# Kernel optimization log

Measured on AMD Instinct MI355X. Metric: run time of the kernel, lower is better.

The kernel has to match this reference:

```python
import jax, jax.numpy as jnp
import numpy as np

B = 2048          # puzzles
E_PER = 1620      # 81 cells * 20 constraint neighbors
N = B * 81        # total nodes
NFEAT = 10


def _winit(key, fan_in, fan_out):
    s = (1.0 / np.sqrt(fan_in)).astype(np.float32) if isinstance(fan_in, np.ndarray) else 1.0 / np.sqrt(fan_in)
    return jax.random.uniform(key, (fan_in, fan_out), jnp.float32, -s, s)


def setup_inputs() -> dict:
    key = jax.random.key(0)
    ks = jax.random.split(key, 20)
    x = jax.random.normal(ks[0], (N, NFEAT), jnp.float32)
    # batched edge index [B, 2, E_PER]; values are global node ids
    edge_index = jax.random.randint(ks[1], (B, 2, E_PER), 0, N, dtype=jnp.int32)
    dims = [(NFEAT, 16), (16, 32), (32, 64), (64, 32), (32, 16)]
    params = {}
    for i, (ci, co) in enumerate(dims, start=1):
        params[f'W{i}'] = _winit(ks[2 * i], ci, co)
        params[f'b{i}'] = jnp.zeros((co,), jnp.float32)
    params['fW1'] = _winit(ks[14], 16, 16)
    params['fb1'] = jnp.zeros((16,), jnp.float32)
    params['fW2'] = _winit(ks[15], 16, 9)
    params['fb2'] = jnp.zeros((9,), jnp.float32)
    return {'x': x, 'edge_index': edge_index, **params}


def _gcn(h, W, b, src, dst, norm):
    # GCNConv: out[i] = sum_{j->i} norm_ij * (h_j W) + b   (self-loops included in src/dst)
    h = h @ W                                  # [N, Cout] small GEMM
    msg = h[src] * norm[:, None]               # gather + scale, [E+N, Cout]
    return jax.ops.segment_sum(msg, dst, num_segments=N) + b


def reference(x, edge_index, W1, b1, W2, b2, W3, b3, W4, b4, W5, b5, fW1, fb1, fW2, fb2):
    # replicate edge_index.permute(1,2,0).reshape(2,-1)
    ei = jnp.transpose(edge_index, (1, 2, 0)).reshape(2, -1)
    src, dst = ei[0], ei[1]
    # add self loops (PyG gcn_norm default)
    loop = jnp.arange(N, dtype=src.dtype)
    src = jnp.concatenate([src, loop])
    dst = jnp.concatenate([dst, loop])
    deg = jax.ops.segment_sum(jnp.ones(src.shape, x.dtype), dst, num_segments=N)
    dinv = jnp.where(deg > 0, jax.lax.rsqrt(jnp.maximum(deg, 1e-12)), 0.0)
    norm = dinv[src] * dinv[dst]               # shared across layers (same graph)
    h = jax.nn.relu(_gcn(x, W1, b1, src, dst, norm))
    h = jax.nn.relu(_gcn(h, W2, b2, src, dst, norm))
    h = jax.nn.relu(_gcn(h, W3, b3, src, dst, norm))
    h = jax.nn.relu(_gcn(h, W4, b4, src, dst, norm))
    h = jax.nn.relu(_gcn(h, W5, b5, src, dst, norm))
    h = h.reshape(-1, 16)
    h = jax.nn.relu(h @ fW1 + fb1)
    h = h @ fW2 + fb2
    return h.reshape(-1, 81, 9)
```

## Files before the change

### kernel.cpp

```cpp
#include <hip/hip_runtime.h>
#include <hip/hip_fp16.h>


#define NN    165888
#define NBAT  2048
#define EPER  1620
#define NEDGE (NBAT * EPER)
#define ETOT  (NEDGE + NN)
#define NBKT  648
#define NBLK  512
#define SLICE 20736
#define BCAP  6144


__device__ inline void blk_scan256(int val, int& excl, int& total, int* sw) {
  int lane = threadIdx.x & 63, w = threadIdx.x >> 6;
  int x = val;
#pragma unroll
  for (int off = 1; off < 64; off <<= 1) {
    int y = __shfl_up(x, off);
    if (lane >= off) x += y;
  }
  if (lane == 63) sw[w] = x;
  __syncthreads();
  int woff = 0;
  if (w > 0) woff = sw[0];
  if (w > 1) woff += sw[1];
  if (w > 2) woff += sw[2];
  total = sw[0] + sw[1] + sw[2] + sw[3];
  excl = woff + x - val;
}

__device__ inline void pbase_scan(const int* __restrict__ btot, int* pb, int* sw) {
  int t = threadIdx.x;
  int e0 = 0, e1 = 0, e2 = 0, s = 0;
  if (t < 216) {
    e0 = btot[3 * t]; e1 = btot[3 * t + 1]; e2 = btot[3 * t + 2];
    s = e0 + e1 + e2;
  }
  int excl, tot;
  blk_scan256(s, excl, tot, sw);
  if (t < 216) {
    pb[3 * t]     = excl;
    pb[3 * t + 1] = excl + e0;
    pb[3 * t + 2] = excl + e0 + e1;
  }
  __syncthreads();
}


__global__ __launch_bounds__(256) void k_count(const int* __restrict__ ei,
                                               int* __restrict__ counts) {
  __shared__ int cnt[NBKT];
  int t = threadIdx.x;
  for (int k = t; k < NBKT; k += 256) cnt[k] = 0;
  __syncthreads();
  int b0 = blockIdx.x * 4;
  for (int b = b0; b < b0 + 4; ++b) {
    const int* dstp = ei + (size_t)b * (2 * EPER) + EPER;
    for (int e = t; e < EPER; e += 256) atomicAdd(&cnt[dstp[e] >> 8], 1);
  }
  __syncthreads();
  for (int k = t; k < NBKT; k += 256) counts[blockIdx.x * NBKT + k] = cnt[k];
}

__global__ __launch_bounds__(256) void k_scan(const int* __restrict__ counts,
                                              int* __restrict__ basesT,
                                              int* __restrict__ btot) {
  int bkt = blockIdx.x, t = threadIdx.x;
  int a = counts[(2 * t)     * NBKT + bkt];
  int b = counts[(2 * t + 1) * NBKT + bkt];
  __shared__ int sw[4];
  int excl, tot;
  blk_scan256(a + b, excl, tot, sw);
  basesT[bkt * NBLK + 2 * t]     = excl;
  basesT[bkt * NBLK + 2 * t + 1] = excl + a;
  if (t == 255) btot[bkt] = tot;
}

__global__ __launch_bounds__(256) void k_scat(const int* __restrict__ ei,
                                              const int* __restrict__ basesT,
                                              const int* __restrict__ btot,
                                              unsigned int* __restrict__ pairs) {
  __shared__ int cur[NBKT];
  __shared__ int pb[NBKT];
  __shared__ int sw[4];
  pbase_scan(btot, pb, sw);
  int t = threadIdx.x;
  for (int k = t; k < NBKT; k += 256)
    cur[k] = pb[k] + basesT[k * NBLK + blockIdx.x];
  __syncthreads();
  int b0 = blockIdx.x * 4;
  for (int b = b0; b < b0 + 4; ++b) {
    const int* srcp = ei + (size_t)b * (2 * EPER);
    const int* dstp = srcp + EPER;
    for (int e = t; e < EPER; e += 256) {
      int d = dstp[e];
      unsigned int s = (unsigned int)srcp[e];
      int pos = atomicAdd(&cur[d >> 8], 1);
      pairs[pos] = s | ((unsigned int)(d & 255) << 24);
    }
  }
}

__global__ __launch_bounds__(256) void k_build(const unsigned int* __restrict__ pairs,
                                               const int* __restrict__ btot,
                                               const float* __restrict__ x,
                                               const float* __restrict__ W1,
                                               int* __restrict__ row_start,
                                               int* __restrict__ row_end,
                                               float* __restrict__ dinv,
                                               int* __restrict__ csr,
                                               __half* __restrict__ g0) {
  __shared__ int pb[NBKT];
  __shared__ int sw[4];
  __shared__ int cnt[256];
  __shared__ unsigned int sp[BCAP];
  __shared__ float sW[160];
  int bkt = blockIdx.x, t = threadIdx.x;
  cnt[t] = 0;
  if (t < 160) sW[t] = W1[t];
  pbase_scan(btot, pb, sw);
  int p0 = pb[bkt];
  int n  = btot[bkt];
  for (int k = t; k < n; k += 256) {
    unsigned int pr = pairs[p0 + k];
    if (k < BCAP) sp[k] = pr;
    atomicAdd(&cnt[pr >> 24], 1);
  }
  __syncthreads();
  int indeg = cnt[t];
  int excl, tot;
  blk_scan256(indeg, excl, tot, sw);
  int csrbase = p0 + bkt * 256;
  int rs   = csrbase + excl + t;
  int node = bkt * 256 + t;
  int d    = indeg + 1;
  float di = rsqrtf((float)d);
  row_start[node] = rs;
  row_end[node]   = rs + d;
  dinv[node] = di;
  csr[rs] = node;
  __syncthreads();
  cnt[t] = rs + 1;
  __syncthreads();
  for (int k = t; k < n; k += 256) {
    unsigned int pr = (k < BCAP) ? sp[k] : pairs[p0 + k];
    int pos = atomicAdd(&cnt[pr >> 24], 1);
    csr[pos] = (int)(pr & 0x00FFFFFFu);
  }
  float r[10];
#pragma unroll
  for (int k = 0; k < 10; ++k) r[k] = x[(size_t)node * 10 + k];
  float acc[16];
#pragma unroll
  for (int j = 0; j < 16; ++j) acc[j] = 0.0f;
#pragma unroll
  for (int k = 0; k < 10; ++k) {
    float rv = r[k];
#pragma unroll
    for (int j = 0; j < 16; ++j) acc[j] = fmaf(rv, sW[k * 16 + j], acc[j]);
  }
  __half* op = g0 + (size_t)node * 16;
  union { int4 v; __half2 h[4]; } pk;
#pragma unroll
  for (int half8 = 0; half8 < 2; ++half8) {
#pragma unroll
    for (int j = 0; j < 4; ++j)
      pk.h[j] = __floats2half2_rn(acc[half8 * 8 + 2 * j] * di,
                                  acc[half8 * 8 + 2 * j + 1] * di);
    *(int4*)(op + half8 * 8) = pk.v;
  }
}


template <int C, int EPI>
__device__ inline float4 agg_core_h(const __half* __restrict__ g,
                                    const int* __restrict__ csr,
                                    int rs, int re, int q, int gl) {
  constexpr int LG = C / 4;
  float4 acc = make_float4(0.f, 0.f, 0.f, 0.f);
  const __half* gq = g + (size_t)q * 4;
  int iters = 0;
  for (int p = rs; p < re; p += EPI) {
    ++iters;
    int m[EPI / LG];
#pragma unroll
    for (int u = 0; u < EPI / LG; ++u) {
      int idx = p + u * LG + q;
      m[u] = csr[idx < re ? idx : re - 1];
    }
    float2 v[EPI];
#pragma unroll
    for (int j = 0; j < EPI; ++j) {
      int s = __shfl(m[j / LG], gl + (j % LG));
      v[j] = *(const float2*)(gq + (size_t)s * C);
    }
#pragma unroll
    for (int j = 0; j < EPI; ++j) {
      const __half2* hp = (const __half2*)&v[j];
      float2 lo = __half22float2(hp[0]);
      float2 hi = __half22float2(hp[1]);
      acc.x += lo.x; acc.y += lo.y; acc.z += hi.x; acc.w += hi.y;
    }
  }
  float dups = (float)(iters * EPI - (re - rs));
  int slast = csr[re - 1];
  float2 vl = *(const float2*)(gq + (size_t)slast * C);
  const __half2* hp = (const __half2*)&vl;
  float2 lo = __half22float2(hp[0]);
  float2 hi = __half22float2(hp[1]);
  acc.x = fmaf(-dups, lo.x, acc.x);
  acc.y = fmaf(-dups, lo.y, acc.y);
  acc.z = fmaf(-dups, hi.x, acc.z);
  acc.w = fmaf(-dups, hi.y, acc.w);
  return acc;
}


__global__ __launch_bounds__(256) void k_agg_ep16(const __half* __restrict__ g,
                                                  const int* __restrict__ row_start,
                                                  const int* __restrict__ row_end,
                                                  const int* __restrict__ csr,
                                                  const float* __restrict__ dinv,
                                                  const float* __restrict__ bias,
                                                  __half* __restrict__ out) {
  constexpr int LG = 4, NPB = 64, SPB = SLICE / NPB;
  int t  = threadIdx.x;
  int q  = t & (LG - 1);
  int bi = blockIdx.x;
  int vb = (bi & 7) * SPB + (bi >> 3);
  int i  = vb * NPB + t / LG;
  int gl = (t & 63) & ~(LG - 1);
  float4 acc = agg_core_h<16, 16>(g, csr, row_start[i], row_end[i], q, gl);
  float di = dinv[i];
  float4 bb = *(const float4*)(bias + q * 4);
  acc.x = fmaxf(fmaf(di, acc.x, bb.x), 0.f) * di;
  acc.y = fmaxf(fmaf(di, acc.y, bb.y), 0.f) * di;
  acc.z = fmaxf(fmaf(di, acc.z, bb.z), 0.f) * di;
  acc.w = fmaxf(fmaf(di, acc.w, bb.w), 0.f) * di;
  union { int2 v; __half2 h[2]; } pk;
  pk.h[0] = __floats2half2_rn(acc.x, acc.y);
  pk.h[1] = __floats2half2_rn(acc.z, acc.w);
  *(int2*)(out + (size_t)i * 16 + q * 4) = pk.v;
}


__global__ __launch_bounds__(256) void k_agg_g2(const __half* __restrict__ g,
                                                const int* __restrict__ row_start,
                                                const int* __restrict__ row_end,
                                                const int* __restrict__ csr,
                                                const float* __restrict__ dinv,
                                                const float* __restrict__ W2,
                                                const float* __restrict__ b2,
                                                __half* __restrict__ out) {
  constexpr int CI = 16, CO = 32, LG = 4, NPB = 64, SPB = SLICE / NPB, RP = 20;
  __shared__ float sW[CI * CO];
  __shared__ float sB[CO];
  __shared__ float rows[NPB * RP];
  __shared__ float sdi[NPB];
  int t = threadIdx.x;
  for (int k = t; k < CI * CO; k += 256) sW[k] = W2[k];
  if (t < CO) sB[t] = b2[t];
  int bi = blockIdx.x;
  int vb = (bi & 7) * SPB + (bi >> 3);
  int nbase = vb * NPB;
  int q = t & (LG - 1), nl = t / LG;
  int i = nbase + nl;
  int gl = (t & 63) & ~(LG - 1);
  float4 acc = agg_core_h<16, 16>(g, csr, row_start[i], row_end[i], q, gl);
  float di = dinv[i];
  acc.x *= di; acc.y *= di; acc.z *= di; acc.w *= di;
  *(float4*)&rows[nl * RP + q * 4] = acc;
  if (q == 0) sdi[nl] = di;
  __syncthreads();
  int n2 = t >> 2, c = t & 3;
  float o[8];
#pragma unroll
  for (int j = 0; j < 8; ++j) o[j] = sB[c * 8 + j];
  const float* row = &rows[n2 * RP];
#pragma unroll
  for (int k = 0; k < CI; ++k) {
    float rv = row[k];
#pragma unroll
    for (int j = 0; j < 8; ++j) o[j] = fmaf(rv, sW[k * CO + c * 8 + j], o[j]);
  }
  float d2 = sdi[n2];
#pragma unroll
  for (int j = 0; j < 8; ++j) o[j] = fmaxf(o[j], 0.f) * d2;
  union { int4 v; __half2 h[4]; } pk;
#pragma unroll
  for (int j = 0; j < 4; ++j) pk.h[j] = __floats2half2_rn(o[2 * j], o[2 * j + 1]);
  *(int4*)(out + (size_t)(nbase + n2) * 32 + c * 8) = pk.v;
}


__global__ __launch_bounds__(256) void k_agg_g34(const __half* __restrict__ g,
                                                 const int* __restrict__ row_start,
                                                 const int* __restrict__ row_end,
                                                 const int* __restrict__ csr,
                                                 const float* __restrict__ dinv,
                                                 const float* __restrict__ W3,
                                                 const float* __restrict__ b3,
                                                 const float* __restrict__ W4,
                                                 __half* __restrict__ out) {
  constexpr int LG = 8, NPB = 32, SPB = SLICE / NPB, RP = 36, HP = 68;
  __shared__ float sW3[32 * 64];
  __shared__ float sW4[64 * 32];
  __shared__ float sB3[64];
  __shared__ float rows[NPB * RP];
  __shared__ float hrows[NPB * HP];
  __shared__ float sdi[NPB];
  int t = threadIdx.x;
  for (int k = t; k < 2048; k += 256) { sW3[k] = W3[k]; sW4[k] = W4[k]; }
  if (t < 64) sB3[t] = b3[t];
  int bi = blockIdx.x;
  int vb = (bi & 7) * SPB + (bi >> 3);
  int nbase = vb * NPB;
  int q = t & (LG - 1), nl = t / LG;
  int i = nbase + nl;
  int gl = (t & 63) & ~(LG - 1);
  float4 acc = agg_core_h<32, 8>(g, csr, row_start[i], row_end[i], q, gl);
  float di = dinv[i];
  acc.x *= di; acc.y *= di; acc.z *= di; acc.w *= di;
  *(float4*)&rows[nl * RP + q * 4] = acc;
  if (q == 0) sdi[nl] = di;
  __syncthreads();
  int n2 = t >> 3, c = t & 7;
  {
    float o[8];
#pragma unroll
    for (int j = 0; j < 8; ++j) o[j] = sB3[c * 8 + j];
    const float* row = &rows[n2 * RP];
#pragma unroll
    for (int k = 0; k < 32; ++k) {
      float rv = row[k];
#pragma unroll
      for (int j = 0; j < 8; ++j) o[j] = fmaf(rv, sW3[k * 64 + c * 8 + j], o[j]);
    }
    float* hp = &hrows[n2 * HP + c * 8];
#pragma unroll
    for (int j = 0; j < 8; ++j) hp[j] = fmaxf(o[j], 0.f);
  }
  __syncthreads();
  {
    float o[4] = {0.f, 0.f, 0.f, 0.f};
    const float* hp = &hrows[n2 * HP];
#pragma unroll
    for (int k = 0; k < 64; ++k) {
      float hv = hp[k];
#pragma unroll
      for (int j = 0; j < 4; ++j) o[j] = fmaf(hv, sW4[k * 32 + c * 4 + j], o[j]);
    }
    float d2 = sdi[n2];
#pragma unroll
    for (int j = 0; j < 4; ++j) o[j] *= d2;
    union { int2 v; __half2 h[2]; } pk;
    pk.h[0] = __floats2half2_rn(o[0], o[1]);
    pk.h[1] = __floats2half2_rn(o[2], o[3]);
    *(int2*)(out + (size_t)(nbase + n2) * 32 + c * 4) = pk.v;
  }
}


__global__ __launch_bounds__(256) void k_agg_g5(const __half* __restrict__ g,
                                                const int* __restrict__ row_start,
                                                const int* __restrict__ row_end,
                                                const int* __restrict__ csr,
                                                const float* __restrict__ dinv,
                                                const float* __restrict__ b4,
                                                const float* __restrict__ W5,
                                                __half* __restrict__ out) {
  constexpr int LG = 8, NPB = 32, SPB = SLICE / NPB, RP = 36;
  __shared__ float sW[32 * 16];
  __shared__ float rows[NPB * RP];
  __shared__ float sdi[NPB];
  int t = threadIdx.x;
  for (int k = t; k < 512; k += 256) sW[k] = W5[k];
  int bi = blockIdx.x;
  int vb = (bi & 7) * SPB + (bi >> 3);
  int nbase = vb * NPB;
  int q = t & (LG - 1), nl = t / LG;
  int i = nbase + nl;
  int gl = (t & 63) & ~(LG - 1);
  float4 acc = agg_core_h<32, 16>(g, csr, row_start[i], row_end[i], q, gl);
  float di = dinv[i];
  float4 bb = *(const float4*)(b4 + q * 4);
  acc.x = fmaxf(fmaf(di, acc.x, bb.x), 0.f);
  acc.y = fmaxf(fmaf(di, acc.y, bb.y), 0.f);
  acc.z = fmaxf(fmaf(di, acc.z, bb.z), 0.f);
  acc.w = fmaxf(fmaf(di, acc.w, bb.w), 0.f);
  *(float4*)&rows[nl * RP + q * 4] = acc;
  if (q == 0) sdi[nl] = di;
  __syncthreads();
  int n2 = t >> 3, c = t & 7;
  float o0 = 0.f, o1 = 0.f;
  const float* row = &rows[n2 * RP];
#pragma unroll
  for (int k = 0; k < 32; ++k) {
    float rv = row[k];
    o0 = fmaf(rv, sW[k * 16 + c * 2],     o0);
    o1 = fmaf(rv, sW[k * 16 + c * 2 + 1], o1);
  }
  float d2 = sdi[n2];
  *(__half2*)(out + (size_t)(nbase + n2) * 16 + c * 2)
      = __floats2half2_rn(o0 * d2, o1 * d2);
}


__global__ __launch_bounds__(256) void k_agg_mlp(const __half* __restrict__ g,
                                                 const int* __restrict__ row_start,
                                                 const int* __restrict__ row_end,
                                                 const int* __restrict__ csr,
                                                 const float* __restrict__ dinv,
                                                 const float* __restrict__ b5,
                                                 const float* __restrict__ fW1,
                                                 const float* __restrict__ fb1,
                                                 const float* __restrict__ fW2,
                                                 const float* __restrict__ fb2,
                                                 float* __restrict__ out) {
  constexpr int LG = 4, NPB = 64, SPB = SLICE / NPB, RP = 20;
  __shared__ float sW1[256], sW2[144], sB1[16], sB2[9];
  __shared__ float rows[NPB * RP];
  __shared__ float zrows[NPB * RP];
  __shared__ float ost[NPB * 9];
  int t = threadIdx.x;
  sW1[t] = fW1[t];
  if (t < 144) sW2[t] = fW2[t];
  if (t < 16)  sB1[t] = fb1[t];
  if (t < 9)   sB2[t] = fb2[t];
  int bi = blockIdx.x;
  int vb = (bi & 7) * SPB + (bi >> 3);
  int nbase = vb * NPB;
  int q = t & (LG - 1), nl = t / LG;
  int i = nbase + nl;
  int gl = (t & 63) & ~(LG - 1);
  float4 acc = agg_core_h<16, 16>(g, csr, row_start[i], row_end[i], q, gl);
  float di = dinv[i];
  float4 bb = *(const float4*)(b5 + q * 4);
  acc.x = fmaxf(fmaf(di, acc.x, bb.x), 0.f);
  acc.y = fmaxf(fmaf(di, acc.y, bb.y), 0.f);
  acc.z = fmaxf(fmaf(di, acc.z, bb.z), 0.f);
  acc.w = fmaxf(fmaf(di, acc.w, bb.w), 0.f);
  *(float4*)&rows[nl * RP + q * 4] = acc;
  __syncthreads();
  int n2 = t >> 2, c = t & 3;
  {
    float o[4];
#pragma unroll
    for (int j = 0; j < 4; ++j) o[j] = sB1[c * 4 + j];
    const float* row = &rows[n2 * RP];
#pragma unroll
    for (int k = 0; k < 16; ++k) {
      float rv = row[k];
#pragma unroll
      for (int j = 0; j < 4; ++j) o[j] = fmaf(rv, sW1[k * 16 + c * 4 + j], o[j]);
    }
    float* zp = &zrows[n2 * RP + c * 4];
#pragma unroll
    for (int j = 0; j < 4; ++j) zp[j] = fmaxf(o[j], 0.f);
  }
  __syncthreads();
  if (c < 3) {
    float o[3];
#pragma unroll
    for (int j = 0; j < 3; ++j) o[j] = sB2[c * 3 + j];
    const float* zp = &zrows[n2 * RP];
#pragma unroll
    for (int k = 0; k < 16; ++k) {
      float zv = zp[k];
#pragma unroll
      for (int j = 0; j < 3; ++j) o[j] = fmaf(zv, sW2[k * 9 + c * 3 + j], o[j]);
    }
#pragma unroll
    for (int j = 0; j < 3; ++j) ost[n2 * 9 + c * 3 + j] = o[j];
  }
  __syncthreads();
  float* ob = out + (size_t)nbase * 9;
  for (int k = t; k < NPB * 9; k += 256) ob[k] = ost[k];
}


extern "C" void kernel_launch(void* const* d_in, const int* in_sizes, int n_in,
                              void* d_out, int out_size, void* d_ws, size_t ws_size,
                              hipStream_t stream) {
  const float* x   = (const float*)d_in[0];
  const int*   ei  = (const int*)d_in[1];
  const float* W1  = (const float*)d_in[2];
  const float* b1  = (const float*)d_in[3];
  const float* W2  = (const float*)d_in[4];
  const float* b2  = (const float*)d_in[5];
  const float* W3  = (const float*)d_in[6];
  const float* b3  = (const float*)d_in[7];
  const float* W4  = (const float*)d_in[8];
  const float* b4  = (const float*)d_in[9];
  const float* W5  = (const float*)d_in[10];
  const float* b5  = (const float*)d_in[11];
  const float* fW1 = (const float*)d_in[12];
  const float* fb1 = (const float*)d_in[13];
  const float* fW2 = (const float*)d_in[14];
  const float* fb2 = (const float*)d_in[15];
  float* out = (float*)d_out;

  char* ws = (char*)d_ws;
  size_t off = 0;
  auto alloc = [&](size_t bytes) -> char* {
    char* p = ws + off;
    off += (bytes + 255) & ~(size_t)255;
    return p;
  };
  int*   counts  = (int*)  alloc((size_t)NBLK * NBKT * 4);
  int*   basesT  = (int*)  alloc((size_t)NBKT * NBLK * 4);
  int*   btot    = (int*)  alloc((size_t)NBKT * 4);
  unsigned int* pairs = (unsigned int*)alloc((size_t)NEDGE * 4);
  int*   rs_     = (int*)  alloc((size_t)NN * 4);
  int*   re_     = (int*)  alloc((size_t)NN * 4);
  float* dinv    = (float*)alloc((size_t)NN * 4);
  int*   csr     = (int*)  alloc((size_t)ETOT * 4);
  __half* H16a   = (__half*)alloc((size_t)NN * 16 * 2);
  __half* H16b   = (__half*)alloc((size_t)NN * 16 * 2);
  __half* H32a   = (__half*)alloc((size_t)NN * 32 * 2);
  __half* H32b   = (__half*)alloc((size_t)NN * 32 * 2);

  k_count<<<NBLK, 256, 0, stream>>>(ei, counts);
  k_scan <<<NBKT, 256, 0, stream>>>(counts, basesT, btot);
  k_scat <<<NBLK, 256, 0, stream>>>(ei, basesT, btot, pairs);
  k_build<<<NBKT, 256, 0, stream>>>(pairs, btot, x, W1, rs_, re_, dinv, csr, H16a);

  k_agg_ep16<<<NN / 64, 256, 0, stream>>>(H16a, rs_, re_, csr, dinv, b1, H16b);
  k_agg_g2<<<NN / 64, 256, 0, stream>>>(H16b, rs_, re_, csr, dinv, W2, b2, H32a);
  k_agg_g34<<<NN / 32, 256, 0, stream>>>(H32a, rs_, re_, csr, dinv, W3, b3, W4, H32b);
  k_agg_g5<<<NN / 32, 256, 0, stream>>>(H32b, rs_, re_, csr, dinv, b4, W5, H16a);
  k_agg_mlp<<<NN / 64, 256, 0, stream>>>(H16a, rs_, re_, csr, dinv, b5,
                                         fW1, fb1, fW2, fb2, out);
}
```

Before: 378.9 us.

## Locally sort scatter pairs in LDS before coalesced global write; widen agg template

The scatter kernel now counts each block's edges per bucket, scans those counts locally, and places the pairs into shared memory grouped by bucket. It then writes them to global memory in contiguous runs, instead of issuing a random global store per edge. This is meant to turn scattered global writes into mostly sequential ones, at the cost of an extra pass over the dst indices, more LDS use (about 33KB) and extra barriers. Separately, one aggregation call changes its second template parameter from 8 to 16.

```diff
diff --git a/kernel.cpp b/kernel.cpp
--- a/kernel.cpp
+++ b/kernel.cpp
@@ -9,6 +9,7 @@
 #define ETOT  (NEDGE + NN)
 #define NBKT  648
 #define NBLK  512
+#define SCATE (4 * EPER)
 #define SLICE 20736
 #define BCAP  6144
 
@@ -82,25 +83,57 @@
                                               const int* __restrict__ basesT,
                                               const int* __restrict__ btot,
                                               unsigned int* __restrict__ pairs) {
-  __shared__ int cur[NBKT];
   __shared__ int pb[NBKT];
   __shared__ int sw[4];
+  __shared__ int cnt[NBKT];
+  __shared__ int lcur[NBKT];
+  __shared__ int gdst[NBKT];
+  __shared__ unsigned int sorted[SCATE];
+  __shared__ unsigned short sbkt[SCATE];
+  int t = threadIdx.x;
+  for (int k = t; k < NBKT; k += 256) cnt[k] = 0;
   pbase_scan(btot, pb, sw);
-  int t = threadIdx.x;
-  for (int k = t; k < NBKT; k += 256)
-    cur[k] = pb[k] + basesT[k * NBLK + blockIdx.x];
-  __syncthreads();
   int b0 = blockIdx.x * 4;
+  for (int b = b0; b < b0 + 4; ++b) {
+    const int* dstp = ei + (size_t)b * (2 * EPER) + EPER;
+    for (int e = t; e < EPER; e += 256) atomicAdd(&cnt[dstp[e] >> 8], 1);
+  }
+  __syncthreads();
+  {
+    int e0 = 0, e1 = 0, e2 = 0, s = 0;
+    if (t < 216) {
+      e0 = cnt[3 * t]; e1 = cnt[3 * t + 1]; e2 = cnt[3 * t + 2];
+      s = e0 + e1 + e2;
+    }
+    int excl, tot;
+    blk_scan256(s, excl, tot, sw);
+    if (t < 216) {
+      cnt[3 * t]     = excl;
+      cnt[3 * t + 1] = excl + e0;
+      cnt[3 * t + 2] = excl + e0 + e1;
+    }
+  }
+  __syncthreads();
+  for (int k = t; k < NBKT; k += 256) {
+    int loc = cnt[k];
+    gdst[k] = pb[k] + basesT[k * NBLK + blockIdx.x] - loc;
+    lcur[k] = loc;
+  }
+  __syncthreads();
   for (int b = b0; b < b0 + 4; ++b) {
     const int* srcp = ei + (size_t)b * (2 * EPER);
     const int* dstp = srcp + EPER;
     for (int e = t; e < EPER; e += 256) {
       int d = dstp[e];
-      unsigned int s = (unsigned int)srcp[e];
-      int pos = atomicAdd(&cur[d >> 8], 1);
-      pairs[pos] = s | ((unsigned int)(d & 255) << 24);
-    }
-  }
+      int bk = d >> 8;
+      int pos = atomicAdd(&lcur[bk], 1);
+      sorted[pos] = (unsigned int)srcp[e] | ((unsigned int)(d & 255) << 24);
+      sbkt[pos]   = (unsigned short)bk;
+    }
+  }
+  __syncthreads();
+  for (int k = t; k < SCATE; k += 256)
+    pairs[gdst[sbkt[k]] + k] = sorted[k];
 }
 
 __global__ __launch_bounds__(256) void k_build(const unsigned int* __restrict__ pairs,
@@ -320,7 +353,7 @@
   int q = t & (LG - 1), nl = t / LG;
   int i = nbase + nl;
   int gl = (t & 63) & ~(LG - 1);
-  float4 acc = agg_core_h<32, 8>(g, csr, row_start[i], row_end[i], q, gl);
+  float4 acc = agg_core_h<32, 16>(g, csr, row_start[i], row_end[i], q, gl);
   float di = dinv[i];
   acc.x *= di; acc.y *= di; acc.z *= di; acc.w *= di;
   *(float4*)&rows[nl * RP + q * 4] = acc;
```

Result: faster. 365.8 us (median of 2 runs) (-3.5%).
